# Optimization experiments

Hardware: AMD Instinct MI355X
Metric: run time of the kernel (lower is better)

## Reference

```python
import jax, jax.numpy as jnp
import numpy as np

D_MODEL = 1024
N_HEADS = 16
D_HEAD = D_MODEL // N_HEADS
N_INS = 3
RANK = 16
EPS = 1e-5


def gelu1p(x):
    # gelu1p feature map: 1 + GELU(x) (positive-ish feature map for linear attention)
    return 1.0 + jax.nn.gelu(x, approximate=False)


def setup_inputs() -> dict:
    key = jax.random.key(0)
    ks = jax.random.split(key, 16)
    B, T = 4, 8192
    x = jax.random.normal(ks[0], (B, T, D_MODEL), dtype=jnp.float32)
    pad_mask = jnp.ones((B, T), dtype=bool)
    s = 1.0 / np.sqrt(D_MODEL)
    wq = jax.random.normal(ks[1], (D_MODEL, D_MODEL), jnp.float32) * s
    wk = jax.random.normal(ks[2], (D_MODEL, D_MODEL), jnp.float32) * s
    wv = jax.random.normal(ks[3], (D_MODEL, D_MODEL), jnp.float32) * s
    wo = jax.random.normal(ks[4], (D_MODEL, D_MODEL), jnp.float32) * s
    sr = 1.0 / np.sqrt(RANK)
    # LoRA weights stacked over insertion points: down (n_ins, rank, d), up (n_ins, d, rank)
    # NOTE: original zero-inits 'up'; we use small random values so LoRA path is exercised.
    def lora(k1, k2):
        return (jax.random.normal(k1, (N_INS, RANK, D_MODEL), jnp.float32) * s,
                jax.random.normal(k2, (N_INS, D_MODEL, RANK), jnp.float32) * sr * 0.01)
    lqd, lqu = lora(ks[5], ks[6])
    lkd, lku = lora(ks[7], ks[8])
    lvd, lvu = lora(ks[9], ks[10])
    lod, lou = lora(ks[11], ks[12])
    return {"x": x, "pad_mask": pad_mask, "insertion_idx": 1,
            "wq": wq, "wk": wk, "wv": wv, "wo": wo,
            "lqd": lqd, "lqu": lqu, "lkd": lkd, "lku": lku,
            "lvd": lvd, "lvu": lvu, "lod": lod, "lou": lou}


def _proj(x, w, down, up):
    # base linear (no bias) + LoRA: x @ w.T + (x @ down.T) @ up.T
    return x @ w.T + (x @ down.T) @ up.T


def reference(x, pad_mask, insertion_idx, wq, wk, wv, wo,
              lqd, lqu, lkd, lku, lvd, lvu, lod, lou):
    B, T, D = x.shape
    i = insertion_idx
    q = _proj(x, wq, lqd[i], lqu[i])
    k = _proj(x, wk, lkd[i], lku[i])
    v = _proj(x, wv, lvd[i], lvu[i])
    # (B, T, H, dh) -> (B, H, T, dh)
    q = q.reshape(B, T, N_HEADS, D_HEAD).transpose(0, 2, 1, 3)
    k = k.reshape(B, T, N_HEADS, D_HEAD).transpose(0, 2, 1, 3)
    v = v.reshape(B, T, N_HEADS, D_HEAD).transpose(0, 2, 1, 3)
    q = gelu1p(q)
    k = gelu1p(k)
    m = pad_mask[:, None, :, None].astype(k.dtype)  # (B,1,T,1)
    k = k * m
    v = v * m
    context = jnp.einsum('bhtd,bhte->bhde', k, v)  # (B,H,dh,dh)
    z = k.sum(axis=-2)                              # (B,H,dh)
    num = jnp.einsum('bhtd,bhde->bhte', q, context)
    den = jnp.einsum('bhtd,bhd->bht', q, z)
    out = num / (den[..., None] + EPS)
    out = out.transpose(0, 2, 1, 3).reshape(B, T, D)
    out = _proj(out, wo, lod[i], lou[i])
    return out
```

## Files before the change

### kernel.cpp

```cpp
#include <hip/hip_runtime.h>
#include <hip/hip_bf16.h>

typedef unsigned short u16;
typedef __attribute__((ext_vector_type(8))) short short8;
typedef __attribute__((ext_vector_type(4))) float f32x4;
typedef __attribute__((ext_vector_type(4))) unsigned short us4;
typedef __attribute__((ext_vector_type(8))) unsigned short us8;

__device__ __forceinline__ u16 f2bf(float f) {
  unsigned int u = __float_as_uint(f);
  u += 0x7fffu + ((u >> 16) & 1u);
  return (u16)(u >> 16);
}
__device__ __forceinline__ float bf2f(u16 h) {
  return __uint_as_float(((unsigned int)h) << 16);
}
__device__ __forceinline__ float gelu1p_f(float x) {
  const float z  = x * 0.7071067811865475f;
  const float az = __builtin_fabsf(z);
  const float t  = __builtin_amdgcn_rcpf(__builtin_fmaf(0.3275911f, az, 1.0f));
  float pl = __builtin_fmaf(1.061405429f, t, -1.453152027f);
  pl = __builtin_fmaf(pl, t, 1.421413741f);
  pl = __builtin_fmaf(pl, t, -0.284496736f);
  pl = __builtin_fmaf(pl, t, 0.254829592f);
  pl = pl * t;
  const float e = __builtin_amdgcn_exp2f(-az * az * 1.4426950408889634f);
  float erfa = __builtin_fmaf(-pl, e, 1.0f);
  erfa = __builtin_copysignf(erfa, z);
  return __builtin_fmaf(x, 0.5f * (1.0f + erfa), 1.0f);
}
__device__ __forceinline__ void gll16(const void* g, void* l) {
  __builtin_amdgcn_global_load_lds(
      (const __attribute__((address_space(1))) unsigned int*)g,
      (__attribute__((address_space(3))) unsigned int*)l, 16, 0, 0);
}
#define FENCE() __builtin_amdgcn_sched_barrier(0)
#define BARRIER() __builtin_amdgcn_s_barrier()
#define LGKM0() do { asm volatile("s_waitcnt lgkmcnt(0)" ::: "memory"); FENCE(); } while (0)
#define VMCNT4() do { asm volatile("s_waitcnt vmcnt(4)" ::: "memory"); FENCE(); } while (0)
#define MFMA16(a, b, c) __builtin_amdgcn_mfma_f32_16x16x32_bf16(a, b, c, 0, 0, 0)

__global__ __launch_bounds__(256)
void build_weff(const float* __restrict__ wq, const float* __restrict__ wk,
                const float* __restrict__ wv, const float* __restrict__ wo,
                const float* __restrict__ lqd, const float* __restrict__ lqu,
                const float* __restrict__ lkd, const float* __restrict__ lku,
                const float* __restrict__ lvd, const float* __restrict__ lvu,
                const float* __restrict__ lod, const float* __restrict__ lou,
                const int* __restrict__ idxp,
                u16* __restrict__ wqkv, u16* __restrict__ wout) {
  const int blk = blockIdx.x;
  const int p = blk >> 10;
  const int n = blk & 1023;
  const int i = *idxp;
  const float* W  = (p == 0) ? wq  : (p == 1) ? wk  : (p == 2) ? wv  : wo;
  const float* Dn = ((p == 0) ? lqd : (p == 1) ? lkd : (p == 2) ? lvd : lod) + (size_t)i * 16 * 1024;
  const float* Up = ((p == 0) ? lqu : (p == 1) ? lku : (p == 2) ? lvu : lou) + (size_t)i * 1024 * 16;

  float up[16];
#pragma unroll
  for (int r = 0; r < 16; ++r) up[r] = Up[n * 16 + r];

  const int k0 = threadIdx.x << 2;
  f32x4 acc = *(const f32x4*)&W[(size_t)n * 1024 + k0];
#pragma unroll
  for (int r = 0; r < 16; ++r) {
    const f32x4 d = *(const f32x4*)&Dn[r * 1024 + k0];
#pragma unroll
    for (int j = 0; j < 4; ++j) acc[j] = __builtin_fmaf(up[r], d[j], acc[j]);
  }
  us4 o;
#pragma unroll
  for (int j = 0; j < 4; ++j) o[j] = f2bf(acc[j]);
  if (p < 3) *(us4*)&wqkv[(size_t)(p * 1024 + n) * 1024 + k0] = o;
  else       *(us4*)&wout[(size_t)n * 1024 + k0] = o;
}

__global__ void xcast(const float* __restrict__ x, u16* __restrict__ xb) {
  const size_t i = ((size_t)blockIdx.x * 256 + threadIdx.x) * 8;
  f32x4 a = *(const f32x4*)(x + i);
  f32x4 b = *(const f32x4*)(x + i + 4);
  us8 o;
#pragma unroll
  for (int j = 0; j < 4; ++j) { o[j] = f2bf(a[j]); o[j + 4] = f2bf(b[j]); }
  *(us8*)(xb + i) = o;
}

template <int MODE>
__global__ __launch_bounds__(512, 2)
void gemm8p(const u16* __restrict__ A, const u16* __restrict__ Bw,
            u16* __restrict__ qb, u16* __restrict__ kbuf, u16* __restrict__ vbuf,
            float* __restrict__ outf, const int* __restrict__ mask, int nbx) {
  const int nwg = gridDim.x;
  const int cpx = nwg >> 3;
  const int xcd = blockIdx.x & 7;
  const int c   = blockIdx.x >> 3;
  const int g   = c / (nbx << 2);
  const int r   = c % (nbx << 2);
  const int bx  = r >> 2;
  const int byi = r & 3;
  const int rows_per_xcd = cpx / nbx;
  const int by  = xcd * rows_per_xcd + (g << 2) + byi;
  const int row0 = by << 8, col0 = bx << 8;
  const int tid = threadIdx.x, lane = tid & 63, w = tid >> 6;
  const int wr = w >> 2, wc = w & 3;

  __shared__ __align__(16) u16 lds[2][2][2][8192];

  const int srow = (w << 4) + (lane & 15);
  const int scol = (lane >> 4) << 3;
  const u16* pA = A  + (size_t)(row0 + srow) * 1024 + scol;
  const u16* pB = Bw + (size_t)(col0 + srow) * 1024 + scol;

  auto stA = [&](int bb, int h, int ts) {
    const u16* s = pA + h * 131072 + ts * 64;
    u16* d = &lds[bb][0][h][((w << 7) + lane) << 3];
    gll16(s, d); gll16(s + 32, d + 512);
  };
  auto stB = [&](int bb, int h, int ts) {
    const u16* s = pB + h * 131072 + ts * 64;
    u16* d = &lds[bb][1][h][((w << 7) + lane) << 3];
    gll16(s, d); gll16(s + 32, d + 512);
  };
  auto LDA = [&](int bb, int m, int kk) {
    return *(const short8*)&lds[bb][0][wr][((((m << 1) | kk) << 6) | lane) << 3];
  };
  auto LDB = [&](int bb, int n, int kk) {
    const int nn = ((wc & 1) << 2) | n;
    return *(const short8*)&lds[bb][1][wc >> 1][((((nn << 1) | kk) << 6) | lane) << 3];
  };

  f32x4 acc[8][4] = {};
  short8 af[4][2], bfv[4][2];

  stA(0, 0, 0); stB(0, 0, 0); stA(0, 1, 0); stB(0, 1, 0);
  stB(1, 0, 1); stA(1, 0, 1);
  VMCNT4();
  BARRIER();

  auto tile = [&](int BUF, int t) {
    const int t1 = (t + 1 < 16) ? t + 1 : 15;
    const int t2 = (t + 2 < 16) ? t + 2 : 15;
#pragma unroll
    for (int m = 0; m < 4; ++m) { af[m][0] = LDA(BUF, m, 0); af[m][1] = LDA(BUF, m, 1); }
#pragma unroll
    for (int n = 0; n < 2; ++n) { bfv[n][0] = LDB(BUF, n, 0); bfv[n][1] = LDB(BUF, n, 1); }
    stA(BUF ^ 1, 1, t1);
    FENCE(); BARRIER(); LGKM0();
    __builtin_amdgcn_s_setprio(1);
#pragma unroll
    for (int m = 0; m < 4; ++m)
#pragma unroll
      for (int n = 0; n < 2; ++n) {
        acc[m][n] = MFMA16(af[m][0], bfv[n][0], acc[m][n]);
        acc[m][n] = MFMA16(af[m][1], bfv[n][1], acc[m][n]);
      }
    __builtin_amdgcn_s_setprio(0);
    FENCE(); BARRIER();
#pragma unroll
    for (int n = 2; n < 4; ++n) { bfv[n][0] = LDB(BUF, n, 0); bfv[n][1] = LDB(BUF, n, 1); }
    stB(BUF ^ 1, 1, t1);
    FENCE(); BARRIER(); LGKM0();
    __builtin_amdgcn_s_setprio(1);
#pragma unroll
    for (int m = 0; m < 4; ++m)
#pragma unroll
      for (int n = 2; n < 4; ++n) {
        acc[m][n] = MFMA16(af[m][0], bfv[n][0], acc[m][n]);
        acc[m][n] = MFMA16(af[m][1], bfv[n][1], acc[m][n]);
      }
    __builtin_amdgcn_s_setprio(0);
    FENCE(); BARRIER();
#pragma unroll
    for (int m = 0; m < 4; ++m) { af[m][0] = LDA(BUF, 4 + m, 0); af[m][1] = LDA(BUF, 4 + m, 1); }
    stB(BUF, 0, t2);
    FENCE(); BARRIER(); LGKM0();
    __builtin_amdgcn_s_setprio(1);
#pragma unroll
    for (int m = 0; m < 4; ++m)
#pragma unroll
      for (int n = 2; n < 4; ++n) {
        acc[4 + m][n] = MFMA16(af[m][0], bfv[n][0], acc[4 + m][n]);
        acc[4 + m][n] = MFMA16(af[m][1], bfv[n][1], acc[4 + m][n]);
      }
    __builtin_amdgcn_s_setprio(0);
    FENCE(); BARRIER();
    stA(BUF, 0, t2);
    FENCE(); BARRIER();
    __builtin_amdgcn_s_setprio(1);
#pragma unroll
    for (int m = 0; m < 4; ++m)
#pragma unroll
      for (int n = 0; n < 2; ++n) {
        acc[4 + m][n] = MFMA16(af[m][0], bfv[n][0], acc[4 + m][n]);
        acc[4 + m][n] = MFMA16(af[m][1], bfv[n][1], acc[4 + m][n]);
      }
    __builtin_amdgcn_s_setprio(0);
    FENCE();
    VMCNT4();
    BARRIER();
  };

#pragma unroll
  for (int it = 0; it < 8; ++it) { tile(0, 2 * it); tile(1, 2 * it + 1); }

  if (MODE == 0) {
    const int cw = col0 + (wc << 6);
    const int p = cw >> 10;
    u16* dst = (p == 0) ? qb : (p == 1) ? kbuf : vbuf;
    const int cc0 = (cw & 1023) + (lane & 15);
#pragma unroll
    for (int m = 0; m < 8; ++m) {
      const int r0 = row0 + (wr << 7) + (m << 4) + ((lane >> 4) << 2);
#pragma unroll
      for (int j = 0; j < 4; ++j) {
        const int r = r0 + j;
        const float mv = (p == 0) ? 1.0f : ((mask[r] != 0) ? 1.0f : 0.0f);
#pragma unroll
        for (int n = 0; n < 4; ++n) {
          float v = acc[m][n][j];
          v = (p == 2) ? v * mv : gelu1p_f(v) * mv;
          dst[(size_t)r * 1024 + cc0 + (n << 4)] = f2bf(v);
        }
      }
    }
  } else {
    const int c0 = col0 + (wc << 6) + (lane & 15);
#pragma unroll
    for (int m = 0; m < 8; ++m) {
      const int r0 = row0 + (wr << 7) + (m << 4) + ((lane >> 4) << 2);
#pragma unroll
      for (int n = 0; n < 4; ++n)
#pragma unroll
        for (int j = 0; j < 4; ++j)
          outf[(size_t)(r0 + j) * 1024 + c0 + (n << 4)] = acc[m][n][j];
    }
  }
}

__global__ __launch_bounds__(64)
void ctx_mfma(const u16* __restrict__ kbuf, const u16* __restrict__ vbuf,
              float* __restrict__ Cpart, float* __restrict__ zpart) {
  const int lane = threadIdx.x;
  const int bh = blockIdx.y, sl = blockIdx.x;
  const int b = bh >> 4, h = bh & 15;
  const size_t base = ((size_t)b * 8192 + (size_t)sl * 512) * 1024 + h * 64;
  const int colA = lane & 15;
  const int tj0 = (lane >> 4) << 3;

  short8 ones;
#pragma unroll
  for (int j = 0; j < 8; ++j) ones[j] = (short)0x3F80;

  f32x4 acc[4][5] = {};

  for (int c = 0; c < 16; ++c) {
    const size_t tbase = base + (size_t)(c * 32 + tj0) * 1024;
    short8 af[4], bv[4];
#pragma unroll
    for (int s = 0; s < 4; ++s) {
      const u16* pk = kbuf + tbase + s * 16 + colA;
      const u16* pv = vbuf + tbase + s * 16 + colA;
      short8 a, v;
#pragma unroll
      for (int j = 0; j < 8; ++j) { a[j] = (short)pk[j * 1024]; v[j] = (short)pv[j * 1024]; }
      af[s] = a; bv[s] = v;
    }
#pragma unroll
    for (int di = 0; di < 4; ++di) {
#pragma unroll
      for (int ei = 0; ei < 4; ++ei)
        acc[di][ei] = MFMA16(af[di], bv[ei], acc[di][ei]);
      acc[di][4] = MFMA16(af[di], ones, acc[di][4]);
    }
  }

  float* cp = Cpart + (size_t)(bh * 16 + sl) * 4096;
  const int el = lane & 15, rb = (lane >> 4) << 2;
#pragma unroll
  for (int di = 0; di < 4; ++di)
#pragma unroll
    for (int j = 0; j < 4; ++j) {
      const int d = di * 16 + rb + j;
#pragma unroll
      for (int ei = 0; ei < 4; ++ei)
        cp[d * 64 + ei * 16 + el] = acc[di][ei][j];
    }
  if (el == 0) {
    float* zp = zpart + (size_t)(bh * 16 + sl) * 64;
#pragma unroll
    for (int di = 0; di < 4; ++di)
#pragma unroll
      for (int j = 0; j < 4; ++j) zp[di * 16 + rb + j] = acc[di][4][j];
  }
}

__global__ void ctx_reduce(const float* __restrict__ Cpart, const float* __restrict__ zpart,
                           u16* __restrict__ Cb) {
  const int bh = blockIdx.x, tid = threadIdx.x;
  for (int idx = tid; idx < 5120; idx += 256) {
    const int d = idx / 80;
    const int e = idx - d * 80;
    float s = 0.f;
    if (e < 64) {
#pragma unroll
      for (int c = 0; c < 16; ++c) s += Cpart[(size_t)(bh * 16 + c) * 4096 + d * 64 + e];
    } else if (e == 64) {
#pragma unroll
      for (int c = 0; c < 16; ++c) s += zpart[(size_t)(bh * 16 + c) * 64 + d];
    }
    Cb[(size_t)bh * 5120 + idx] = f2bf(s);
  }
}

__global__ __launch_bounds__(256)
void attn_out(const u16* __restrict__ qbuf, const u16* __restrict__ Cb,
              u16* __restrict__ ratio) {
  const int tid = threadIdx.x, lane = tid & 63, wave = tid >> 6;
  const int bh = blockIdx.y, b = bh >> 4, h = bh & 15;
  const int t0 = blockIdx.x * 256 + wave * 64;
  const size_t mbase = (size_t)b * 8192;
  const u16* cb = Cb + (size_t)bh * 5120;

  short8 bfrag[5][2];
#pragma unroll
  for (int nt = 0; nt < 5; ++nt)
#pragma unroll
    for (int kf = 0; kf < 2; ++kf) {
      short8 f;
#pragma unroll
      for (int j = 0; j < 8; ++j) {
        const int d = kf * 32 + ((lane >> 4) << 3) + j;
        f[j] = (short)cb[d * 80 + nt * 16 + (lane & 15)];
      }
      bfrag[nt][kf] = f;
    }

  f32x4 acc[4][5] = {};
#pragma unroll
  for (int mt = 0; mt < 4; ++mt) {
    const int tr = t0 + mt * 16 + (lane & 15);
    const u16* qrow = qbuf + (mbase + tr) * 1024 + h * 64 + ((lane >> 4) << 3);
    short8 a0 = *(const short8*)qrow;
    short8 a1 = *(const short8*)(qrow + 32);
#pragma unroll
    for (int nt = 0; nt < 5; ++nt) {
      acc[mt][nt] = MFMA16(a0, bfrag[nt][0], acc[mt][nt]);
      acc[mt][nt] = MFMA16(a1, bfrag[nt][1], acc[mt][nt]);
    }
  }

#pragma unroll
  for (int mt = 0; mt < 4; ++mt) {
#pragma unroll
    for (int j = 0; j < 4; ++j) {
      const float den = __shfl(acc[mt][4][j], lane & 48, 64);
      const float inv = 1.0f / (den + 1e-5f);
      const int tr = t0 + mt * 16 + ((lane >> 4) << 2) + j;
      u16* orow = ratio + (mbase + tr) * 1024 + h * 64;
#pragma unroll
      for (int nt = 0; nt < 4; ++nt)
        orow[nt * 16 + (lane & 15)] = f2bf(acc[mt][nt][j] * inv);
    }
  }
}

extern "C" void kernel_launch(void* const* d_in, const int* in_sizes, int n_in,
                              void* d_out, int out_size, void* d_ws, size_t ws_size,
                              hipStream_t stream) {
  (void)in_sizes; (void)n_in; (void)out_size; (void)ws_size;
  const float* x = (const float*)d_in[0];
  const int* mask = (const int*)d_in[1];
  const int* idx = (const int*)d_in[2];
  const float* wq = (const float*)d_in[3];
  const float* wk = (const float*)d_in[4];
  const float* wv = (const float*)d_in[5];
  const float* wo = (const float*)d_in[6];
  const float* lqd = (const float*)d_in[7];
  const float* lqu = (const float*)d_in[8];
  const float* lkd = (const float*)d_in[9];
  const float* lku = (const float*)d_in[10];
  const float* lvd = (const float*)d_in[11];
  const float* lvu = (const float*)d_in[12];
  const float* lod = (const float*)d_in[13];
  const float* lou = (const float*)d_in[14];
  float* out = (float*)d_out;

  char* ws = (char*)d_ws;
  u16* xb    = (u16*)ws;
  u16* wqkv  = (u16*)(ws + (64ll << 20));
  u16* wo_b  = (u16*)(ws + (70ll << 20));
  u16* qb    = (u16*)(ws + (72ll << 20));
  u16* kb    = (u16*)(ws + (136ll << 20));
  u16* vb    = (u16*)(ws + (200ll << 20));
  float* Cpart = (float*)ws;
  float* zpart = (float*)(ws + (272ll << 20));
  u16* Cb    = (u16*)(ws + (273ll << 20));
  u16* ratio = xb;

  build_weff<<<dim3(4096), dim3(256), 0, stream>>>(wq, wk, wv, wo,
      lqd, lqu, lkd, lku, lvd, lvu, lod, lou, idx, wqkv, wo_b);
  xcast<<<dim3(16384), dim3(256), 0, stream>>>(x, xb);
  gemm8p<0><<<dim3(1536), dim3(512), 0, stream>>>(xb, wqkv, qb, kb, vb, nullptr, mask, 12);
  ctx_mfma<<<dim3(16, 64), dim3(64), 0, stream>>>(kb, vb, Cpart, zpart);
  ctx_reduce<<<dim3(64), dim3(256), 0, stream>>>(Cpart, zpart, Cb);
  attn_out<<<dim3(32, 64), dim3(256), 0, stream>>>(qb, Cb, ratio);
  gemm8p<1><<<dim3(512), dim3(512), 0, stream>>>(ratio, wo_b, nullptr, nullptr, nullptr, out, mask, 4);
}
```

Before: 487.9 us.

## Switch GEMM inner loop to 32x32x16 MFMA with relaid LDS and finer waitcnts

Replaces the 16x16x32 bf16 MFMA tiling of the main projection GEMM with 32x32x16 MFMAs, reorganising the global-to-LDS staging layout and fragment loads to match. Several intra-phase barriers are replaced by partial lgkmcnt waits so MFMAs can start while later LDS reads are still in flight. The epilogue is rewritten for the 32x32 accumulator layout. The larger MFMA shape cuts instruction issue and LDS read traffic per FLOP, but it changes register pressure and the LDS bank access pattern, and dropping barriers adds risk of data hazards.

```diff
diff --git a/kernel.cpp b/kernel.cpp
--- a/kernel.cpp
+++ b/kernel.cpp
@@ -4,6 +4,7 @@
 typedef unsigned short u16;
 typedef __attribute__((ext_vector_type(8))) short short8;
 typedef __attribute__((ext_vector_type(4))) float f32x4;
+typedef __attribute__((ext_vector_type(16))) float f32x16;
 typedef __attribute__((ext_vector_type(4))) unsigned short us4;
 typedef __attribute__((ext_vector_type(8))) unsigned short us8;
 
@@ -36,9 +37,10 @@
 }
 #define FENCE() __builtin_amdgcn_sched_barrier(0)
 #define BARRIER() __builtin_amdgcn_s_barrier()
-#define LGKM0() do { asm volatile("s_waitcnt lgkmcnt(0)" ::: "memory"); FENCE(); } while (0)
-#define VMCNT4() do { asm volatile("s_waitcnt vmcnt(4)" ::: "memory"); FENCE(); } while (0)
+#define LGKM(n) do { asm volatile("s_waitcnt lgkmcnt(" #n ")" ::: "memory"); FENCE(); } while (0)
+#define VMCNT(n) do { asm volatile("s_waitcnt vmcnt(" #n ")" ::: "memory"); FENCE(); } while (0)
 #define MFMA16(a, b, c) __builtin_amdgcn_mfma_f32_16x16x32_bf16(a, b, c, 0, 0, 0)
+#define MFMA32(a, b, c) __builtin_amdgcn_mfma_f32_32x32x16_bf16(a, b, c, 0, 0, 0)
 
 __global__ __launch_bounds__(256)
 void build_weff(const float* __restrict__ wq, const float* __restrict__ wk,
@@ -107,133 +109,163 @@
 
   __shared__ __align__(16) u16 lds[2][2][2][8192];
 
-  const int srow = (w << 4) + (lane & 15);
-  const int scol = (lane >> 4) << 3;
-  const u16* pA = A  + (size_t)(row0 + srow) * 1024 + scol;
-  const u16* pB = Bw + (size_t)(col0 + srow) * 1024 + scol;
+  int goff[2];
+#pragma unroll
+  for (int cc = 0; cc < 2; ++cc) {
+    const int sub = cc * 512 + tid;
+    const int f = sub >> 6, l = sub & 63;
+    goff[cc] = ((f >> 2) * 32 + (l & 31)) * 1024 + (f & 3) * 16 + ((l >> 5) << 3);
+  }
+  const u16* pA = A  + (size_t)row0 * 1024;
+  const u16* pB = Bw + (size_t)col0 * 1024;
 
   auto stA = [&](int bb, int h, int ts) {
     const u16* s = pA + h * 131072 + ts * 64;
-    u16* d = &lds[bb][0][h][((w << 7) + lane) << 3];
-    gll16(s, d); gll16(s + 32, d + 512);
+    gll16(s + goff[0], &lds[bb][0][h][tid << 3]);
+    gll16(s + goff[1], &lds[bb][0][h][(512 + tid) << 3]);
   };
   auto stB = [&](int bb, int h, int ts) {
     const u16* s = pB + h * 131072 + ts * 64;
-    u16* d = &lds[bb][1][h][((w << 7) + lane) << 3];
-    gll16(s, d); gll16(s + 32, d + 512);
+    gll16(s + goff[0], &lds[bb][1][h][tid << 3]);
+    gll16(s + goff[1], &lds[bb][1][h][(512 + tid) << 3]);
   };
-  auto LDA = [&](int bb, int m, int kk) {
-    return *(const short8*)&lds[bb][0][wr][((((m << 1) | kk) << 6) | lane) << 3];
+  auto LDA = [&](int bb, int rg, int kg) {
+    return *(const short8*)&lds[bb][0][wr][(((rg << 2) | kg) << 9) + (lane << 3)];
   };
-  auto LDB = [&](int bb, int n, int kk) {
-    const int nn = ((wc & 1) << 2) | n;
-    return *(const short8*)&lds[bb][1][wc >> 1][((((nn << 1) | kk) << 6) | lane) << 3];
+  auto LDB = [&](int bb, int cg, int kg) {
+    const int f = ((((wc & 1) << 1) | cg) << 2) | kg;
+    return *(const short8*)&lds[bb][1][wc >> 1][(f << 9) + (lane << 3)];
   };
 
-  f32x4 acc[8][4] = {};
-  short8 af[4][2], bfv[4][2];
+  f32x16 acc[4][2] = {};
+  short8 af[2][4], bf[2][4];
 
   stA(0, 0, 0); stB(0, 0, 0); stA(0, 1, 0); stB(0, 1, 0);
   stB(1, 0, 1); stA(1, 0, 1);
-  VMCNT4();
+  VMCNT(4);
   BARRIER();
 
   auto tile = [&](int BUF, int t) {
     const int t1 = (t + 1 < 16) ? t + 1 : 15;
     const int t2 = (t + 2 < 16) ? t + 2 : 15;
-#pragma unroll
-    for (int m = 0; m < 4; ++m) { af[m][0] = LDA(BUF, m, 0); af[m][1] = LDA(BUF, m, 1); }
-#pragma unroll
-    for (int n = 0; n < 2; ++n) { bfv[n][0] = LDB(BUF, n, 0); bfv[n][1] = LDB(BUF, n, 1); }
+    af[0][0] = LDA(BUF, 0, 0); af[1][0] = LDA(BUF, 1, 0);
+    bf[0][0] = LDB(BUF, 0, 0); bf[1][0] = LDB(BUF, 1, 0);
+    FENCE();
+    af[0][1] = LDA(BUF, 0, 1); af[1][1] = LDA(BUF, 1, 1);
+    bf[0][1] = LDB(BUF, 0, 1); bf[1][1] = LDB(BUF, 1, 1);
     stA(BUF ^ 1, 1, t1);
-    FENCE(); BARRIER(); LGKM0();
+    FENCE();
+    LGKM(4);
     __builtin_amdgcn_s_setprio(1);
-#pragma unroll
-    for (int m = 0; m < 4; ++m)
-#pragma unroll
-      for (int n = 0; n < 2; ++n) {
-        acc[m][n] = MFMA16(af[m][0], bfv[n][0], acc[m][n]);
-        acc[m][n] = MFMA16(af[m][1], bfv[n][1], acc[m][n]);
-      }
+    acc[0][0] = MFMA32(af[0][0], bf[0][0], acc[0][0]);
+    acc[0][1] = MFMA32(af[0][0], bf[1][0], acc[0][1]);
+    acc[1][0] = MFMA32(af[1][0], bf[0][0], acc[1][0]);
+    acc[1][1] = MFMA32(af[1][0], bf[1][0], acc[1][1]);
+    LGKM(0);
+    acc[0][0] = MFMA32(af[0][1], bf[0][1], acc[0][0]);
+    acc[0][1] = MFMA32(af[0][1], bf[1][1], acc[0][1]);
+    acc[1][0] = MFMA32(af[1][1], bf[0][1], acc[1][0]);
+    acc[1][1] = MFMA32(af[1][1], bf[1][1], acc[1][1]);
     __builtin_amdgcn_s_setprio(0);
     FENCE(); BARRIER();
-#pragma unroll
-    for (int n = 2; n < 4; ++n) { bfv[n][0] = LDB(BUF, n, 0); bfv[n][1] = LDB(BUF, n, 1); }
+    af[0][2] = LDA(BUF, 0, 2); af[1][2] = LDA(BUF, 1, 2);
+    bf[0][2] = LDB(BUF, 0, 2); bf[1][2] = LDB(BUF, 1, 2);
+    FENCE();
+    af[0][3] = LDA(BUF, 0, 3); af[1][3] = LDA(BUF, 1, 3);
+    bf[0][3] = LDB(BUF, 0, 3); bf[1][3] = LDB(BUF, 1, 3);
     stB(BUF ^ 1, 1, t1);
-    FENCE(); BARRIER(); LGKM0();
+    FENCE();
+    LGKM(4);
     __builtin_amdgcn_s_setprio(1);
-#pragma unroll
-    for (int m = 0; m < 4; ++m)
-#pragma unroll
-      for (int n = 2; n < 4; ++n) {
-        acc[m][n] = MFMA16(af[m][0], bfv[n][0], acc[m][n]);
-        acc[m][n] = MFMA16(af[m][1], bfv[n][1], acc[m][n]);
-      }
+    acc[0][0] = MFMA32(af[0][2], bf[0][2], acc[0][0]);
+    acc[0][1] = MFMA32(af[0][2], bf[1][2], acc[0][1]);
+    acc[1][0] = MFMA32(af[1][2], bf[0][2], acc[1][0]);
+    acc[1][1] = MFMA32(af[1][2], bf[1][2], acc[1][1]);
+    LGKM(0);
+    acc[0][0] = MFMA32(af[0][3], bf[0][3], acc[0][0]);
+    acc[0][1] = MFMA32(af[0][3], bf[1][3], acc[0][1]);
+    acc[1][0] = MFMA32(af[1][3], bf[0][3], acc[1][0]);
+    acc[1][1] = MFMA32(af[1][3], bf[1][3], acc[1][1]);
     __builtin_amdgcn_s_setprio(0);
     FENCE(); BARRIER();
-#pragma unroll
-    for (int m = 0; m < 4; ++m) { af[m][0] = LDA(BUF, 4 + m, 0); af[m][1] = LDA(BUF, 4 + m, 1); }
+    af[0][0] = LDA(BUF, 2, 0); af[1][0] = LDA(BUF, 3, 0);
+    FENCE();
+    af[0][1] = LDA(BUF, 2, 1); af[1][1] = LDA(BUF, 3, 1);
+    FENCE();
+    af[0][2] = LDA(BUF, 2, 2); af[1][2] = LDA(BUF, 3, 2);
+    af[0][3] = LDA(BUF, 2, 3); af[1][3] = LDA(BUF, 3, 3);
     stB(BUF, 0, t2);
-    FENCE(); BARRIER(); LGKM0();
+    FENCE();
+    LGKM(6);
     __builtin_amdgcn_s_setprio(1);
-#pragma unroll
-    for (int m = 0; m < 4; ++m)
-#pragma unroll
-      for (int n = 2; n < 4; ++n) {
-        acc[4 + m][n] = MFMA16(af[m][0], bfv[n][0], acc[4 + m][n]);
-        acc[4 + m][n] = MFMA16(af[m][1], bfv[n][1], acc[4 + m][n]);
-      }
+    acc[2][0] = MFMA32(af[0][0], bf[0][0], acc[2][0]);
+    acc[2][1] = MFMA32(af[0][0], bf[1][0], acc[2][1]);
+    acc[3][0] = MFMA32(af[1][0], bf[0][0], acc[3][0]);
+    acc[3][1] = MFMA32(af[1][0], bf[1][0], acc[3][1]);
+    LGKM(4);
+    acc[2][0] = MFMA32(af[0][1], bf[0][1], acc[2][0]);
+    acc[2][1] = MFMA32(af[0][1], bf[1][1], acc[2][1]);
+    acc[3][0] = MFMA32(af[1][1], bf[0][1], acc[3][0]);
+    acc[3][1] = MFMA32(af[1][1], bf[1][1], acc[3][1]);
     __builtin_amdgcn_s_setprio(0);
-    FENCE(); BARRIER();
+    FENCE();
+    LGKM(0);
+    BARRIER();
     stA(BUF, 0, t2);
-    FENCE(); BARRIER();
+    FENCE();
     __builtin_amdgcn_s_setprio(1);
-#pragma unroll
-    for (int m = 0; m < 4; ++m)
-#pragma unroll
-      for (int n = 0; n < 2; ++n) {
-        acc[4 + m][n] = MFMA16(af[m][0], bfv[n][0], acc[4 + m][n]);
-        acc[4 + m][n] = MFMA16(af[m][1], bfv[n][1], acc[4 + m][n]);
-      }
+    acc[2][0] = MFMA32(af[0][2], bf[0][2], acc[2][0]);
+    acc[2][1] = MFMA32(af[0][2], bf[1][2], acc[2][1]);
+    acc[3][0] = MFMA32(af[1][2], bf[0][2], acc[3][0]);
+    acc[3][1] = MFMA32(af[1][2], bf[1][2], acc[3][1]);
+    acc[2][0] = MFMA32(af[0][3], bf[0][3], acc[2][0]);
+    acc[2][1] = MFMA32(af[0][3], bf[1][3], acc[2][1]);
+    acc[3][0] = MFMA32(af[1][3], bf[0][3], acc[3][0]);
+    acc[3][1] = MFMA32(af[1][3], bf[1][3], acc[3][1]);
     __builtin_amdgcn_s_setprio(0);
     FENCE();
-    VMCNT4();
+    VMCNT(4);
     BARRIER();
   };
 
 #pragma unroll
   for (int it = 0; it < 8; ++it) { tile(0, 2 * it); tile(1, 2 * it + 1); }
+  VMCNT(0);
 
   if (MODE == 0) {
-    const int cw = col0 + (wc << 6);
-    const int p = cw >> 10;
+    const int p = col0 >> 10;
     u16* dst = (p == 0) ? qb : (p == 1) ? kbuf : vbuf;
-    const int cc0 = (cw & 1023) + (lane & 15);
-#pragma unroll
-    for (int m = 0; m < 8; ++m) {
-      const int r0 = row0 + (wr << 7) + (m << 4) + ((lane >> 4) << 2);
-#pragma unroll
-      for (int j = 0; j < 4; ++j) {
-        const int r = r0 + j;
-        const float mv = (p == 0) ? 1.0f : ((mask[r] != 0) ? 1.0f : 0.0f);
-#pragma unroll
-        for (int n = 0; n < 4; ++n) {
-          float v = acc[m][n][j];
+    const int ccb = (col0 & 1023) + (wc << 6) + (lane & 31);
+#pragma unroll
+    for (int rg = 0; rg < 4; ++rg) {
+      const int r00 = row0 + (wr << 7) + (rg << 5) + ((lane >> 5) << 2);
+#pragma unroll
+      for (int cg = 0; cg < 2; ++cg) {
+        const int cc = ccb + (cg << 5);
+#pragma unroll
+        for (int reg = 0; reg < 16; ++reg) {
+          const int rr = r00 + (reg & 3) + ((reg >> 2) << 3);
+          const float mv = (p == 0) ? 1.0f : ((mask[rr] != 0) ? 1.0f : 0.0f);
+          float v = acc[rg][cg][reg];
           v = (p == 2) ? v * mv : gelu1p_f(v) * mv;
-          dst[(size_t)r * 1024 + cc0 + (n << 4)] = f2bf(v);
+          dst[(size_t)rr * 1024 + cc] = f2bf(v);
         }
       }
     }
   } else {
-    const int c0 = col0 + (wc << 6) + (lane & 15);
-#pragma unroll
-    for (int m = 0; m < 8; ++m) {
-      const int r0 = row0 + (wr << 7) + (m << 4) + ((lane >> 4) << 2);
-#pragma unroll
-      for (int n = 0; n < 4; ++n)
-#pragma unroll
-        for (int j = 0; j < 4; ++j)
-          outf[(size_t)(r0 + j) * 1024 + c0 + (n << 4)] = acc[m][n][j];
+    const int ccb = col0 + (wc << 6) + (lane & 31);
+#pragma unroll
+    for (int rg = 0; rg < 4; ++rg) {
+      const int r00 = row0 + (wr << 7) + (rg << 5) + ((lane >> 5) << 2);
+#pragma unroll
+      for (int cg = 0; cg < 2; ++cg) {
+        const int cc = ccb + (cg << 5);
+#pragma unroll
+        for (int reg = 0; reg < 16; ++reg) {
+          const int rr = r00 + (reg & 3) + ((reg >> 2) << 3);
+          outf[(size_t)rr * 1024 + cc] = acc[rg][cg][reg];
+        }
+      }
     }
   }
 }
```

Result: slower. 543.0 us (+11.3%).
